# Kernel optimization log

Measured on AMD Instinct MI355X. Metric: run time of the kernel, lower is better.

## Reference

```python
import jax, jax.numpy as jnp
import numpy as np

HIDDEN = 1024
HEADS = 16
HEAD_DIM = HIDDEN // HEADS


def setup_inputs() -> dict:
    key = jax.random.key(0)
    k1, k2, k3, k4 = jax.random.split(key, 4)
    x = jax.random.normal(k1, (4, 2048, HIDDEN), dtype=jnp.float32)
    # qkv: Linear(hidden, 3*hidden, bias=False) -> weight [3*hidden, hidden]
    w_qkv = jax.random.normal(k2, (3 * HIDDEN, HIDDEN), dtype=jnp.float32) * (HIDDEN ** -0.5)
    # out_proj: Linear(hidden, hidden) with bias
    w_out = jax.random.normal(k3, (HIDDEN, HIDDEN), dtype=jnp.float32) * (HIDDEN ** -0.5)
    b_out = jax.random.normal(k4, (HIDDEN,), dtype=jnp.float32) * 0.01
    return {"x": x, "w_qkv": w_qkv, "w_out": w_out, "b_out": b_out}


def reference(x, w_qkv, w_out, b_out):
    B, N, _ = x.shape
    scale = HEAD_DIM ** -0.5
    qkv = jnp.einsum('bnc,dc->bnd', x, w_qkv)            # [B,N,3*hidden]
    qkv = qkv.reshape(B, N, 3, HEADS, HEAD_DIM)
    qkv = jnp.transpose(qkv, (2, 0, 3, 1, 4))            # [3,B,H,N,hd]
    q, k, v = qkv[0], qkv[1], qkv[2]
    att = jnp.einsum('bhxd,bhyd->bhxy', q, k) * scale    # [B,H,N,N]
    att = jax.nn.softmax(att, axis=-1)
    out = jnp.einsum('bhxy,bhyd->bhxd', att, v)          # [B,H,N,hd]
    out = jnp.transpose(out, (0, 2, 1, 3)).reshape(B, N, HIDDEN)
    out = jnp.einsum('bnc,dc->bnd', out, w_out) + b_out
    return out
```

## Files before the change

kernel.cpp:

```cpp
#include <hip/hip_runtime.h>

typedef unsigned short u16;
typedef short short8 __attribute__((ext_vector_type(8)));
typedef float f32x4 __attribute__((ext_vector_type(4)));
typedef float f32x16 __attribute__((ext_vector_type(16)));
typedef unsigned short u16x4 __attribute__((ext_vector_type(4)));
typedef unsigned int u32x4 __attribute__((ext_vector_type(4)));

#define MFMA16(a, b, c) __builtin_amdgcn_mfma_f32_16x16x32_bf16((a), (b), (c), 0, 0, 0)
#define MFMA32(a, b, c) __builtin_amdgcn_mfma_f32_32x32x16_bf16((a), (b), (c), 0, 0, 0)

#if __has_builtin(__builtin_amdgcn_exp2f)
#define EXP2F(x) __builtin_amdgcn_exp2f(x)
#else
#define EXP2F(x) exp2f(x)
#endif

__device__ __forceinline__ u16 f2bf(float f) {
    unsigned u = __builtin_bit_cast(unsigned, f);
    u += 0x7FFFu + ((u >> 16) & 1u);
    return (u16)(u >> 16);
}

__device__ __forceinline__ void async16(void* lds, const void* g) {
    __builtin_amdgcn_global_load_lds(
        (const __attribute__((address_space(1))) void*)g,
        (__attribute__((address_space(3))) void*)lds, 16, 0, 0);
}

__device__ __forceinline__ unsigned cvtpk(float lo, float hi) {
    unsigned r;
    asm("v_cvt_pk_bf16_f32 %0, %1, %2" : "=v"(r) : "v"(lo), "v"(hi));
    return r;
}
__device__ __forceinline__ void plswap(unsigned& a, unsigned& b) {
    asm("v_permlane32_swap_b32 %0, %1" : "+v"(a), "+v"(b));
}

__device__ __forceinline__ void packP(const f32x16& s, short8& f0, short8& f1) {
    u32x4 u0, u1;
    {
        unsigned a = cvtpk(s[0], s[1]), b = cvtpk(s[4], s[5]);
        plswap(a, b);
        unsigned c = cvtpk(s[2], s[3]), d = cvtpk(s[6], s[7]);
        plswap(c, d);
        u0[0] = a; u0[1] = c; u0[2] = b; u0[3] = d;
    }
    {
        unsigned a = cvtpk(s[8], s[9]), b = cvtpk(s[12], s[13]);
        plswap(a, b);
        unsigned c = cvtpk(s[10], s[11]), d = cvtpk(s[14], s[15]);
        plswap(c, d);
        u1[0] = a; u1[1] = c; u1[2] = b; u1[3] = d;
    }
    f0 = __builtin_bit_cast(short8, u0);
    f1 = __builtin_bit_cast(short8, u1);
}

__global__ __launch_bounds__(256) void cast3(const float* __restrict__ x,
                                             const float* __restrict__ wqkv,
                                             const float* __restrict__ wout,
                                             u16* __restrict__ dst) {
    const int blk = blockIdx.x;
    const float* src;
    int idx;
    float sc = 1.0f;
    u16* out;
    if (blk < 8192) {
        src = x; out = dst; idx = (blk * 256 + threadIdx.x) * 4;
    } else if (blk < 11264) {
        src = wqkv; out = dst + (size_t)8192 * 1024;
        idx = ((blk - 8192) * 256 + threadIdx.x) * 4;
        if (idx < 1024 * 1024) sc = 0.18033688011112042f;
    } else {
        src = wout; out = dst + (size_t)11264 * 1024;
        idx = ((blk - 11264) * 256 + threadIdx.x) * 4;
    }
    float4 v = *(const float4*)(src + idx);
    u16x4 r;
    r[0] = f2bf(v.x * sc); r[1] = f2bf(v.y * sc);
    r[2] = f2bf(v.z * sc); r[3] = f2bf(v.w * sc);
    *(u16x4*)(out + idx) = r;
}

__global__ __launch_bounds__(512, 2) void gemm256(const u16* __restrict__ A,
                                                  const u16* __restrict__ B,
                                                  u16* __restrict__ qk) {
    __shared__ u16 lds[2][2][16384];
    const int tid = threadIdx.x;
    const int l = tid & 63;
    const int w = tid >> 6;
    const int g = l >> 4, lo = l & 15;
    const int wrow = w >> 2, wcol = w & 3;
    const int xcd = blockIdx.x & 7, j = blockIdx.x >> 3;
    const int tm = xcd * 4 + (j & 3), tn = j >> 2;
    const int rowBase = tm << 8, colBase = tn << 8;

    const int srow = tid >> 3;
    const int scol = (((tid * 16) ^ (((tid >> 3) & 7) << 4)) & 127) >> 1;
    const u16* pa = A + (size_t)(rowBase + srow) * 1024 + scol;
    const u16* pb = B + (size_t)(colBase + srow) * 1024 + scol;
    const int ldsOff = tid * 16;

    int abase[2], bbase[2];
#pragma unroll
    for (int k = 0; k < 2; ++k) {
        abase[k] = (((wrow * 128 + lo) * 128 + k * 64 + g * 16) ^ ((lo & 7) << 4));
        bbase[k] = (((wcol * 64 + lo) * 128 + k * 64 + g * 16) ^ ((lo & 7) << 4));
    }

    f32x4 acc[8][4] = {};

#define STAGE256(buf, kt)                                                                   \
    {                                                                                       \
        const u16* sa = pa + (kt) * 64;                                                     \
        const u16* sb = pb + (kt) * 64;                                                     \
        _Pragma("unroll")                                                                   \
        for (int i = 0; i < 4; ++i) {                                                       \
            async16((char*)lds[buf][0] + ldsOff + i * 8192, sa + (size_t)i * 64 * 1024);    \
            async16((char*)lds[buf][1] + ldsOff + i * 8192, sb + (size_t)i * 64 * 1024);    \
        }                                                                                   \
    }

    STAGE256(0, 0);
    __syncthreads();

    for (int kt = 0; kt < 16; ++kt) {
        const int cur = kt & 1;
        if (kt < 15) STAGE256(cur ^ 1, kt + 1);
        const char* la = (const char*)lds[cur][0];
        const char* lb = (const char*)lds[cur][1];

        short8 bf[4][2], af[4][2];
#pragma unroll
        for (int n = 0; n < 4; ++n)
#pragma unroll
            for (int k = 0; k < 2; ++k)
                bf[n][k] = *(const short8*)(lb + bbase[k] + n * 2048);
#pragma unroll
        for (int m = 0; m < 4; ++m)
#pragma unroll
            for (int k = 0; k < 2; ++k)
                af[m][k] = *(const short8*)(la + abase[k] + m * 2048);
        __builtin_amdgcn_s_setprio(1);
#pragma unroll
        for (int m = 0; m < 4; ++m)
#pragma unroll
            for (int n = 0; n < 4; ++n) {
                acc[m][n] = MFMA16(af[m][0], bf[n][0], acc[m][n]);
                acc[m][n] = MFMA16(af[m][1], bf[n][1], acc[m][n]);
            }
        __builtin_amdgcn_s_setprio(0);
#pragma unroll
        for (int m = 0; m < 4; ++m)
#pragma unroll
            for (int k = 0; k < 2; ++k)
                af[m][k] = *(const short8*)(la + abase[k] + (m + 4) * 2048);
        __builtin_amdgcn_s_setprio(1);
#pragma unroll
        for (int m = 0; m < 4; ++m)
#pragma unroll
            for (int n = 0; n < 4; ++n) {
                acc[m + 4][n] = MFMA16(af[m][0], bf[n][0], acc[m + 4][n]);
                acc[m + 4][n] = MFMA16(af[m][1], bf[n][1], acc[m + 4][n]);
            }
        __builtin_amdgcn_s_setprio(0);
        __syncthreads();
    }
#undef STAGE256

#pragma unroll
    for (int n = 0; n < 4; ++n) {
        const int c = colBase + wcol * 64 + n * 16 + lo;
#pragma unroll
        for (int m = 0; m < 8; ++m) {
            const int r0 = rowBase + wrow * 128 + m * 16 + g * 4;
#pragma unroll
            for (int i = 0; i < 4; ++i)
                qk[(size_t)(r0 + i) * 2048 + c] = f2bf(acc[m][n][i]);
        }
    }
}

__global__ __launch_bounds__(256, 2) void gemmV(const u16* __restrict__ A,
                                                const u16* __restrict__ Bv,
                                                u16* __restrict__ vt) {
    __shared__ u16 As[128 * 64];
    __shared__ u16 Bs[128 * 64];
    const int tid = threadIdx.x;
    const int w = tid >> 6, l = tid & 63;
    const int g = l >> 4, lo = l & 15;
    const int xcd = blockIdx.x & 7, j = blockIdx.x >> 3;
    const int tm = xcd * 8 + (j & 7), tn = j >> 3;
    const int rowBase = tm << 7, colBase = tn << 7;
    const int wrow = w >> 1, wcol = w & 1;

    const int srow = tid >> 3;
    const int scol = (((tid * 16) ^ (((tid >> 3) & 7) << 4)) & 127) >> 1;
    const u16* pa = A + (size_t)(rowBase + srow) * 1024 + scol;
    const u16* pb = Bv + (size_t)(colBase + srow) * 1024 + scol;
    const int ldsOff = tid * 16;

    int abase[2], bbase[2];
#pragma unroll
    for (int k = 0; k < 2; ++k) {
        abase[k] = (((wrow * 64 + lo) * 128 + k * 64 + g * 16) ^ ((lo & 7) << 4));
        bbase[k] = (((wcol * 64 + lo) * 128 + k * 64 + g * 16) ^ ((lo & 7) << 4));
    }

    f32x4 acc[4][4] = {};

    for (int kt = 0; kt < 16; ++kt) {
        const int kbase = kt * 64;
#pragma unroll
        for (int i = 0; i < 4; ++i) {
            async16((char*)As + ldsOff + i * 4096, pa + kbase + (size_t)i * 32 * 1024);
            async16((char*)Bs + ldsOff + i * 4096, pb + kbase + (size_t)i * 32 * 1024);
        }
        __syncthreads();
        short8 af[4][2], bf[4][2];
#pragma unroll
        for (int mi = 0; mi < 4; ++mi)
#pragma unroll
            for (int k = 0; k < 2; ++k)
                af[mi][k] = *(const short8*)((const char*)As + abase[k] + mi * 2048);
#pragma unroll
        for (int ni = 0; ni < 4; ++ni)
#pragma unroll
            for (int k = 0; k < 2; ++k)
                bf[ni][k] = *(const short8*)((const char*)Bs + bbase[k] + ni * 2048);
        __builtin_amdgcn_s_setprio(1);
#pragma unroll
        for (int mi = 0; mi < 4; ++mi)
#pragma unroll
            for (int ni = 0; ni < 4; ++ni) {
                acc[mi][ni] = MFMA16(af[mi][0], bf[ni][0], acc[mi][ni]);
                acc[mi][ni] = MFMA16(af[mi][1], bf[ni][1], acc[mi][ni]);
            }
        __builtin_amdgcn_s_setprio(0);
        __syncthreads();
    }

    const int b = rowBase >> 11;
#pragma unroll
    for (int ni = 0; ni < 4; ++ni) {
        const int c = colBase + wcol * 64 + ni * 16 + lo;
        const int hh = c >> 6, d = c & 63;
        u16* vrow = vt + ((size_t)((b * 16 + hh) * 64 + d)) * 2048;
#pragma unroll
        for (int mi = 0; mi < 4; ++mi) {
            const int r0 = rowBase + wrow * 64 + mi * 16 + g * 4;
            u16x4 pk;
#pragma unroll
            for (int i = 0; i < 4; ++i) pk[i] = f2bf(acc[mi][ni][i]);
            *(u16x4*)(vrow + (r0 & 2047)) = pk;
        }
    }
}

__global__ __launch_bounds__(256, 2) void gemm_bt(const u16* __restrict__ A,
                                                  const u16* __restrict__ B,
                                                  float* __restrict__ Cf,
                                                  const float* __restrict__ bias,
                                                  int M, int N, int K) {
    __shared__ u16 As[128 * 64];
    __shared__ u16 Bs[128 * 64];
    const int tid = threadIdx.x;
    const int w = tid >> 6, l = tid & 63;
    const int g = l >> 4, lo = l & 15;
    const int mtiles = M >> 7;
    const int S = mtiles >> 3;
    const int xcd = blockIdx.x & 7, j = blockIdx.x >> 3;
    const int tm = xcd * S + (j % S), tn = j / S;
    const int rowBase = tm << 7, colBase = tn << 7;
    const int wrow = w >> 1, wcol = w & 1;

    const int srow = tid >> 3;
    const int scol = (((tid * 16) ^ (((tid >> 3) & 7) << 4)) & 127) >> 1;
    const u16* pa = A + (size_t)(rowBase + srow) * K + scol;
    const u16* pb = B + (size_t)(colBase + srow) * K + scol;
    const int ldsOff = tid * 16;

    int abase[2], bbase[2];
#pragma unroll
    for (int k = 0; k < 2; ++k) {
        abase[k] = (((wrow * 64 + lo) * 128 + k * 64 + g * 16) ^ ((lo & 7) << 4));
        bbase[k] = (((wcol * 64 + lo) * 128 + k * 64 + g * 16) ^ ((lo & 7) << 4));
    }

    f32x4 acc[4][4] = {};

    const int nk = K >> 6;
    for (int kt = 0; kt < nk; ++kt) {
        const int kbase = kt * 64;
#pragma unroll
        for (int i = 0; i < 4; ++i) {
            async16((char*)As + ldsOff + i * 4096, pa + kbase + (size_t)i * 32 * K);
            async16((char*)Bs + ldsOff + i * 4096, pb + kbase + (size_t)i * 32 * K);
        }
        __syncthreads();
        short8 af[4][2], bf[4][2];
#pragma unroll
        for (int mi = 0; mi < 4; ++mi)
#pragma unroll
            for (int k = 0; k < 2; ++k)
                af[mi][k] = *(const short8*)((const char*)As + abase[k] + mi * 2048);
#pragma unroll
        for (int ni = 0; ni < 4; ++ni)
#pragma unroll
            for (int k = 0; k < 2; ++k)
                bf[ni][k] = *(const short8*)((const char*)Bs + bbase[k] + ni * 2048);
        __builtin_amdgcn_s_setprio(1);
#pragma unroll
        for (int mi = 0; mi < 4; ++mi)
#pragma unroll
            for (int ni = 0; ni < 4; ++ni) {
                acc[mi][ni] = MFMA16(af[mi][0], bf[ni][0], acc[mi][ni]);
                acc[mi][ni] = MFMA16(af[mi][1], bf[ni][1], acc[mi][ni]);
            }
        __builtin_amdgcn_s_setprio(0);
        __syncthreads();
    }

#pragma unroll
    for (int ni = 0; ni < 4; ++ni) {
        const int c = colBase + wcol * 64 + ni * 16 + lo;
        const float bv = bias[c];
#pragma unroll
        for (int mi = 0; mi < 4; ++mi) {
            const int r0 = rowBase + wrow * 64 + mi * 16 + g * 4;
#pragma unroll
            for (int i = 0; i < 4; ++i)
                Cf[(size_t)(r0 + i) * N + c] = acc[mi][ni][i] + bv;
        }
    }
}

__global__ __launch_bounds__(256, 2) void attn_fwd(const u16* __restrict__ qkb,
                                                   const u16* __restrict__ vtg,
                                                   u16* __restrict__ outb) {
    __shared__ u16 Ks[2][2][4096];
    __shared__ u16 Vs[2][2][4096];
    const int tid = threadIdx.x;
    const int w = tid >> 6, l = tid & 63;
    const int hi = l >> 5, lq = l & 31;

    const int lin = (blockIdx.x & 7) * 64 + (blockIdx.x >> 3);
    const int bh = lin >> 3, qt = lin & 7;
    const int b = bh >> 4, h = bh & 15;
    const size_t rowQ0 = (size_t)b * 2048 + qt * 256 + w * 32;
    const size_t rowQ1 = rowQ0 + 128;

    short8 qf0[4], qf1[4];
#pragma unroll
    for (int ks = 0; ks < 4; ++ks) {
        qf0[ks] = *(const short8*)(qkb + (rowQ0 + lq) * 2048 + h * 64 + ks * 16 + hi * 8);
        qf1[ks] = *(const short8*)(qkb + (rowQ1 + lq) * 2048 + h * 64 + ks * 16 + hi * 8);
    }

    int koff[4];
#pragma unroll
    for (int ks = 0; ks < 4; ++ks)
        koff[ks] = (lq * 128 + ks * 32 + hi * 16) ^ ((lq & 7) << 4);

    const int L0 = tid * 16, L1 = tid * 16 + 4096;
    const int kr0 = L0 >> 7, kc0 = ((L0 ^ ((kr0 & 7) << 4)) & 127) >> 1;
    const int kr1 = L1 >> 7, kc1 = ((L1 ^ ((kr1 & 7) << 4)) & 127) >> 1;
    const u16* ks0 = qkb + (size_t)(b * 2048 + kr0) * 2048 + 1024 + h * 64 + kc0;
    const u16* ks1 = qkb + (size_t)(b * 2048 + kr1) * 2048 + 1024 + h * 64 + kc1;
    const u16* vs0 = vtg + ((size_t)bh * 64 + kr0) * 2048 + kc0;
    const u16* vs1 = vtg + ((size_t)bh * 64 + kr1) * 2048 + kc1;
    const size_t KADV = (size_t)128 * 2048;
    const size_t CADV = (size_t)64 * 2048;

    f32x16 O00, O01, Ol0, O10, O11, Ol1;
#pragma unroll
    for (int i = 0; i < 16; ++i) {
        O00[i] = 0.f; O01[i] = 0.f; Ol0[i] = 0.f;
        O10[i] = 0.f; O11[i] = 0.f; Ol1[i] = 0.f;
    }
    const f32x16 Z = {};
    const short8 onesv = {16256, 16256, 16256, 16256, 16256, 16256, 16256, 16256};

#define STAGEKV(buf)                                                        \
    {                                                                       \
        async16((char*)Ks[buf][0] + L0, ks0);                               \
        async16((char*)Ks[buf][0] + L1, ks1);                               \
        async16((char*)Ks[buf][1] + L0, ks0 + CADV);                        \
        async16((char*)Ks[buf][1] + L1, ks1 + CADV);                        \
        async16((char*)Vs[buf][0] + L0, vs0);                               \
        async16((char*)Vs[buf][0] + L1, vs1);                               \
        async16((char*)Vs[buf][1] + L0, vs0 + 64);                          \
        async16((char*)Vs[buf][1] + L1, vs1 + 64);                          \
        ks0 += KADV; ks1 += KADV; vs0 += 128; vs1 += 128;                   \
    }

    STAGEKV(0);

    int cur = 0;
    for (int kt = 0; kt < 16; ++kt) {
        __syncthreads();
        if (kt < 15) STAGEKV(cur ^ 1);

#pragma unroll
        for (int c = 0; c < 2; ++c) {
            const char* kb = (const char*)Ks[cur][c];
            const char* vb = (const char*)Vs[cur][c];

#pragma unroll
            for (int t = 0; t < 2; ++t) {
                const int tb = t * 4096;
                short8 kf0 = *(const short8*)(kb + koff[0] + tb);
                short8 kf1 = *(const short8*)(kb + koff[1] + tb);
                short8 kf2 = *(const short8*)(kb + koff[2] + tb);
                short8 kf3 = *(const short8*)(kb + koff[3] + tb);
                short8 vfa = *(const short8*)(vb + koff[t * 2]);
                short8 vfb = *(const short8*)(vb + koff[t * 2] + 4096);
                short8 vfc = *(const short8*)(vb + koff[t * 2 + 1]);
                short8 vfd = *(const short8*)(vb + koff[t * 2 + 1] + 4096);

                {
                    __builtin_amdgcn_s_setprio(1);
                    f32x16 s = MFMA32(kf0, qf0[0], Z);
                    s = MFMA32(kf1, qf0[1], s);
                    s = MFMA32(kf2, qf0[2], s);
                    s = MFMA32(kf3, qf0[3], s);
                    __builtin_amdgcn_s_setprio(0);
#pragma unroll
                    for (int i = 0; i < 16; ++i) s[i] = EXP2F(s[i]);
                    short8 p0, p1;
                    packP(s, p0, p1);
                    __builtin_amdgcn_s_setprio(1);
                    Ol0 = MFMA32(p0, onesv, Ol0);
                    Ol0 = MFMA32(p1, onesv, Ol0);
                    O00 = MFMA32(p0, vfa, O00);
                    O01 = MFMA32(p0, vfb, O01);
                    O00 = MFMA32(p1, vfc, O00);
                    O01 = MFMA32(p1, vfd, O01);
                    __builtin_amdgcn_s_setprio(0);
                }
                {
                    __builtin_amdgcn_s_setprio(1);
                    f32x16 s = MFMA32(kf0, qf1[0], Z);
                    s = MFMA32(kf1, qf1[1], s);
                    s = MFMA32(kf2, qf1[2], s);
                    s = MFMA32(kf3, qf1[3], s);
                    __builtin_amdgcn_s_setprio(0);
#pragma unroll
                    for (int i = 0; i < 16; ++i) s[i] = EXP2F(s[i]);
                    short8 p0, p1;
                    packP(s, p0, p1);
                    __builtin_amdgcn_s_setprio(1);
                    Ol1 = MFMA32(p0, onesv, Ol1);
                    Ol1 = MFMA32(p1, onesv, Ol1);
                    O10 = MFMA32(p0, vfa, O10);
                    O11 = MFMA32(p0, vfb, O11);
                    O10 = MFMA32(p1, vfc, O10);
                    O11 = MFMA32(p1, vfd, O11);
                    __builtin_amdgcn_s_setprio(0);
                }
            }
        }
        cur ^= 1;
    }
#undef STAGEKV

#pragma unroll
    for (int r = 0; r < 16; ++r) {
        const int qrow = (r & 3) + 8 * (r >> 2) + 4 * hi;
        {
            const float linv = 1.0f / Ol0[r];
            u16* op = outb + (rowQ0 + qrow) * 1024 + h * 64 + lq;
            op[0] = f2bf(O00[r] * linv);
            op[32] = f2bf(O01[r] * linv);
        }
        {
            const float linv = 1.0f / Ol1[r];
            u16* op = outb + (rowQ1 + qrow) * 1024 + h * 64 + lq;
            op[0] = f2bf(O10[r] * linv);
            op[32] = f2bf(O11[r] * linv);
        }
    }
}

extern "C" void kernel_launch(void* const* d_in, const int* in_sizes, int n_in,
                              void* d_out, int out_size, void* d_ws, size_t ws_size,
                              hipStream_t stream) {
    const float* x     = (const float*)d_in[0];
    const float* w_qkv = (const float*)d_in[1];
    const float* w_out = (const float*)d_in[2];
    const float* b_out = (const float*)d_in[3];
    float* out = (float*)d_out;

    u16* xb    = (u16*)d_ws;
    u16* wqkvb = xb    + (size_t)8192 * 1024;
    u16* woutb = wqkvb + (size_t)3072 * 1024;
    u16* qkb   = woutb + (size_t)1024 * 1024;
    u16* vtg   = qkb   + (size_t)8192 * 2048;
    u16* attb  = vtg   + (size_t)64 * 64 * 2048;

    cast3<<<12288, 256, 0, stream>>>(x, w_qkv, w_out, xb);

    gemm256<<<256, 512, 0, stream>>>(xb, wqkvb, qkb);
    gemmV<<<512, 256, 0, stream>>>(xb, wqkvb + (size_t)2048 * 1024, vtg);

    attn_fwd<<<512, 256, 0, stream>>>(qkb, vtg, attb);

    gemm_bt<<<dim3((8192 / 128) * (1024 / 128)), 256, 0, stream>>>(
        attb, woutb, out, b_out, 8192, 1024, 1024);
}
```

Baseline: 170.8 us.

## Merge Q/K and V projections into one double-buffered 128x128 GEMM kernel

Replaces the separate 256x256 QK GEMM and 128x128 V GEMM with a single 1536-block 128x128 kernel. It branches in the epilogue to write either the row-major QK output or the transposed V layout. The unified QKV kernel and the output-projection GEMM now double-buffer their LDS tiles, so the next K-slice loads while the current one computes. This removes a kernel launch and the per-iteration load stall, but smaller tiles lower the arithmetic intensity for the QK part and double the LDS per block.

After: 173.8 us. No clear change (+1.8%).

```diff
diff --git a/kernel.cpp b/kernel.cpp
--- a/kernel.cpp
+++ b/kernel.cpp
@@ -83,110 +83,12 @@
     *(u16x4*)(out + idx) = r;
 }
 
-__global__ __launch_bounds__(512, 2) void gemm256(const u16* __restrict__ A,
+__global__ __launch_bounds__(256, 2) void gemmQKV(const u16* __restrict__ A,
                                                   const u16* __restrict__ B,
-                                                  u16* __restrict__ qk) {
-    __shared__ u16 lds[2][2][16384];
-    const int tid = threadIdx.x;
-    const int l = tid & 63;
-    const int w = tid >> 6;
-    const int g = l >> 4, lo = l & 15;
-    const int wrow = w >> 2, wcol = w & 3;
-    const int xcd = blockIdx.x & 7, j = blockIdx.x >> 3;
-    const int tm = xcd * 4 + (j & 3), tn = j >> 2;
-    const int rowBase = tm << 8, colBase = tn << 8;
-
-    const int srow = tid >> 3;
-    const int scol = (((tid * 16) ^ (((tid >> 3) & 7) << 4)) & 127) >> 1;
-    const u16* pa = A + (size_t)(rowBase + srow) * 1024 + scol;
-    const u16* pb = B + (size_t)(colBase + srow) * 1024 + scol;
-    const int ldsOff = tid * 16;
-
-    int abase[2], bbase[2];
-#pragma unroll
-    for (int k = 0; k < 2; ++k) {
-        abase[k] = (((wrow * 128 + lo) * 128 + k * 64 + g * 16) ^ ((lo & 7) << 4));
-        bbase[k] = (((wcol * 64 + lo) * 128 + k * 64 + g * 16) ^ ((lo & 7) << 4));
-    }
-
-    f32x4 acc[8][4] = {};
-
-#define STAGE256(buf, kt)                                                                   \
-    {                                                                                       \
-        const u16* sa = pa + (kt) * 64;                                                     \
-        const u16* sb = pb + (kt) * 64;                                                     \
-        _Pragma("unroll")                                                                   \
-        for (int i = 0; i < 4; ++i) {                                                       \
-            async16((char*)lds[buf][0] + ldsOff + i * 8192, sa + (size_t)i * 64 * 1024);    \
-            async16((char*)lds[buf][1] + ldsOff + i * 8192, sb + (size_t)i * 64 * 1024);    \
-        }                                                                                   \
-    }
-
-    STAGE256(0, 0);
-    __syncthreads();
-
-    for (int kt = 0; kt < 16; ++kt) {
-        const int cur = kt & 1;
-        if (kt < 15) STAGE256(cur ^ 1, kt + 1);
-        const char* la = (const char*)lds[cur][0];
-        const char* lb = (const char*)lds[cur][1];
-
-        short8 bf[4][2], af[4][2];
-#pragma unroll
-        for (int n = 0; n < 4; ++n)
-#pragma unroll
-            for (int k = 0; k < 2; ++k)
-                bf[n][k] = *(const short8*)(lb + bbase[k] + n * 2048);
-#pragma unroll
-        for (int m = 0; m < 4; ++m)
-#pragma unroll
-            for (int k = 0; k < 2; ++k)
-                af[m][k] = *(const short8*)(la + abase[k] + m * 2048);
-        __builtin_amdgcn_s_setprio(1);
-#pragma unroll
-        for (int m = 0; m < 4; ++m)
-#pragma unroll
-            for (int n = 0; n < 4; ++n) {
-                acc[m][n] = MFMA16(af[m][0], bf[n][0], acc[m][n]);
-                acc[m][n] = MFMA16(af[m][1], bf[n][1], acc[m][n]);
-            }
-        __builtin_amdgcn_s_setprio(0);
-#pragma unroll
-        for (int m = 0; m < 4; ++m)
-#pragma unroll
-            for (int k = 0; k < 2; ++k)
-                af[m][k] = *(const short8*)(la + abase[k] + (m + 4) * 2048);
-        __builtin_amdgcn_s_setprio(1);
-#pragma unroll
-        for (int m = 0; m < 4; ++m)
-#pragma unroll
-            for (int n = 0; n < 4; ++n) {
-                acc[m + 4][n] = MFMA16(af[m][0], bf[n][0], acc[m + 4][n]);
-                acc[m + 4][n] = MFMA16(af[m][1], bf[n][1], acc[m + 4][n]);
-            }
-        __builtin_amdgcn_s_setprio(0);
-        __syncthreads();
-    }
-#undef STAGE256
-
-#pragma unroll
-    for (int n = 0; n < 4; ++n) {
-        const int c = colBase + wcol * 64 + n * 16 + lo;
-#pragma unroll
-        for (int m = 0; m < 8; ++m) {
-            const int r0 = rowBase + wrow * 128 + m * 16 + g * 4;
-#pragma unroll
-            for (int i = 0; i < 4; ++i)
-                qk[(size_t)(r0 + i) * 2048 + c] = f2bf(acc[m][n][i]);
-        }
-    }
-}
-
-__global__ __launch_bounds__(256, 2) void gemmV(const u16* __restrict__ A,
-                                                const u16* __restrict__ Bv,
-                                                u16* __restrict__ vt) {
-    __shared__ u16 As[128 * 64];
-    __shared__ u16 Bs[128 * 64];
+                                                  u16* __restrict__ qk,
+                                                  u16* __restrict__ vt) {
+    __shared__ u16 As[2][128 * 64];
+    __shared__ u16 Bs[2][128 * 64];
     const int tid = threadIdx.x;
     const int w = tid >> 6, l = tid & 63;
     const int g = l >> 4, lo = l & 15;
@@ -198,7 +100,7 @@
     const int srow = tid >> 3;
     const int scol = (((tid * 16) ^ (((tid >> 3) & 7) << 4)) & 127) >> 1;
     const u16* pa = A + (size_t)(rowBase + srow) * 1024 + scol;
-    const u16* pb = Bv + (size_t)(colBase + srow) * 1024 + scol;
+    const u16* pb = B + (size_t)(colBase + srow) * 1024 + scol;
     const int ldsOff = tid * 16;
 
     int abase[2], bbase[2];
@@ -210,25 +112,36 @@
 
     f32x4 acc[4][4] = {};
 
+#define STAGEQKV(buf, kt)                                                                  \
+    {                                                                                      \
+        const int kb_ = (kt) * 64;                                                         \
+        _Pragma("unroll")                                                                  \
+        for (int i = 0; i < 4; ++i) {                                                      \
+            async16((char*)As[buf] + ldsOff + i * 4096, pa + kb_ + (size_t)i * 32 * 1024); \
+            async16((char*)Bs[buf] + ldsOff + i * 4096, pb + kb_ + (size_t)i * 32 * 1024); \
+        }                                                                                  \
+    }
+
+    STAGEQKV(0, 0);
+    __syncthreads();
+
     for (int kt = 0; kt < 16; ++kt) {
-        const int kbase = kt * 64;
-#pragma unroll
-        for (int i = 0; i < 4; ++i) {
-            async16((char*)As + ldsOff + i * 4096, pa + kbase + (size_t)i * 32 * 1024);
-            async16((char*)Bs + ldsOff + i * 4096, pb + kbase + (size_t)i * 32 * 1024);
-        }
-        __syncthreads();
+        const int cur = kt & 1;
+        if (kt < 15) STAGEQKV(cur ^ 1, kt + 1);
+        const char* la = (const char*)As[cur];
+        const char* lb = (const char*)Bs[cur];
+
         short8 af[4][2], bf[4][2];
 #pragma unroll
         for (int mi = 0; mi < 4; ++mi)
 #pragma unroll
             for (int k = 0; k < 2; ++k)
-                af[mi][k] = *(const short8*)((const char*)As + abase[k] + mi * 2048);
+                af[mi][k] = *(const short8*)(la + abase[k] + mi * 2048);
 #pragma unroll
         for (int ni = 0; ni < 4; ++ni)
 #pragma unroll
             for (int k = 0; k < 2; ++k)
-                bf[ni][k] = *(const short8*)((const char*)Bs + bbase[k] + ni * 2048);
+                bf[ni][k] = *(const short8*)(lb + bbase[k] + ni * 2048);
         __builtin_amdgcn_s_setprio(1);
 #pragma unroll
         for (int mi = 0; mi < 4; ++mi)
@@ -240,20 +153,35 @@
         __builtin_amdgcn_s_setprio(0);
         __syncthreads();
     }
-
-    const int b = rowBase >> 11;
-#pragma unroll
-    for (int ni = 0; ni < 4; ++ni) {
-        const int c = colBase + wcol * 64 + ni * 16 + lo;
-        const int hh = c >> 6, d = c & 63;
-        u16* vrow = vt + ((size_t)((b * 16 + hh) * 64 + d)) * 2048;
-#pragma unroll
-        for (int mi = 0; mi < 4; ++mi) {
-            const int r0 = rowBase + wrow * 64 + mi * 16 + g * 4;
-            u16x4 pk;
-#pragma unroll
-            for (int i = 0; i < 4; ++i) pk[i] = f2bf(acc[mi][ni][i]);
-            *(u16x4*)(vrow + (r0 & 2047)) = pk;
+#undef STAGEQKV
+
+    if (colBase < 2048) {
+#pragma unroll
+        for (int ni = 0; ni < 4; ++ni) {
+            const int c = colBase + wcol * 64 + ni * 16 + lo;
+#pragma unroll
+            for (int mi = 0; mi < 4; ++mi) {
+                const int r0 = rowBase + wrow * 64 + mi * 16 + g * 4;
+#pragma unroll
+                for (int i = 0; i < 4; ++i)
+                    qk[(size_t)(r0 + i) * 2048 + c] = f2bf(acc[mi][ni][i]);
+            }
+        }
+    } else {
+        const int b = rowBase >> 11;
+#pragma unroll
+        for (int ni = 0; ni < 4; ++ni) {
+            const int c = colBase + wcol * 64 + ni * 16 + lo;
+            const int hh = (c - 2048) >> 6, d = (c - 2048) & 63;
+            u16* vrow = vt + ((size_t)((b * 16 + hh) * 64 + d)) * 2048;
+#pragma unroll
+            for (int mi = 0; mi < 4; ++mi) {
+                const int r0 = rowBase + wrow * 64 + mi * 16 + g * 4;
+                u16x4 pk;
+#pragma unroll
+                for (int i = 0; i < 4; ++i) pk[i] = f2bf(acc[mi][ni][i]);
+                *(u16x4*)(vrow + (r0 & 2047)) = pk;
+            }
         }
     }
 }
@@ -263,8 +191,8 @@
                                                   float* __restrict__ Cf,
                                                   const float* __restrict__ bias,
                                                   int M, int N, int K) {
-    __shared__ u16 As[128 * 64];
-    __shared__ u16 Bs[128 * 64];
+    __shared__ u16 As[2][128 * 64];
+    __shared__ u16 Bs[2][128 * 64];
     const int tid = threadIdx.x;
     const int w = tid >> 6, l = tid & 63;
     const int g = l >> 4, lo = l & 15;
@@ -290,26 +218,37 @@
 
     f32x4 acc[4][4] = {};
 
+#define STAGE2(buf, kt)                                                                 \
+    {                                                                                   \
+        const int kb_ = (kt) * 64;                                                      \
+        _Pragma("unroll")                                                               \
+        for (int i = 0; i < 4; ++i) {                                                   \
+            async16((char*)As[buf] + ldsOff + i * 4096, pa + kb_ + (size_t)i * 32 * K); \
+            async16((char*)Bs[buf] + ldsOff + i * 4096, pb + kb_ + (size_t)i * 32 * K); \
+        }                                                                               \
+    }
+
     const int nk = K >> 6;
+    STAGE2(0, 0);
+    __syncthreads();
+
     for (int kt = 0; kt < nk; ++kt) {
-        const int kbase = kt * 64;
-#pragma unroll
-        for (int i = 0; i < 4; ++i) {
-            async16((char*)As + ldsOff + i * 4096, pa + kbase + (size_t)i * 32 * K);
-            async16((char*)Bs + ldsOff + i * 4096, pb + kbase + (size_t)i * 32 * K);
-        }
-        __syncthreads();
+        const int cur = kt & 1;
+        if (kt < nk - 1) STAGE2(cur ^ 1, kt + 1);
+        const char* la = (const char*)As[cur];
+        const char* lb = (const char*)Bs[cur];
+
         short8 af[4][2], bf[4][2];
 #pragma unroll
         for (int mi = 0; mi < 4; ++mi)
 #pragma unroll
             for (int k = 0; k < 2; ++k)
-                af[mi][k] = *(const short8*)((const char*)As + abase[k] + mi * 2048);
+                af[mi][k] = *(const short8*)(la + abase[k] + mi * 2048);
 #pragma unroll
         for (int ni = 0; ni < 4; ++ni)
 #pragma unroll
             for (int k = 0; k < 2; ++k)
-                bf[ni][k] = *(const short8*)((const char*)Bs + bbase[k] + ni * 2048);
+                bf[ni][k] = *(const short8*)(lb + bbase[k] + ni * 2048);
         __builtin_amdgcn_s_setprio(1);
 #pragma unroll
         for (int mi = 0; mi < 4; ++mi)
@@ -321,6 +260,7 @@
         __builtin_amdgcn_s_setprio(0);
         __syncthreads();
     }
+#undef STAGE2
 
 #pragma unroll
     for (int ni = 0; ni < 4; ++ni) {
@@ -501,11 +441,10 @@
 
     cast3<<<12288, 256, 0, stream>>>(x, w_qkv, w_out, xb);
 
-    gemm256<<<256, 512, 0, stream>>>(xb, wqkvb, qkb);
-    gemmV<<<512, 256, 0, stream>>>(xb, wqkvb + (size_t)2048 * 1024, vtg);
+    gemmQKV<<<1536, 256, 0, stream>>>(xb, wqkvb, qkb, vtg);
 
     attn_fwd<<<512, 256, 0, stream>>>(qkb, vtg, attb);
 
-    gemm_bt<<<dim3((8192 / 128) * (1024 / 128)), 256, 0, stream>>>(
+    gemm_bt<<<dim3(512), 256, 0, stream>>>(
         attb, woutb, out, b_out, 8192, 1024, 1024);
 }
```

## Replace 256x256 double-buffered QK GEMM with 128x128 single-buffered tiles

Applied to the files above, without the earlier changes.

The Q/K projection GEMM goes from 256x256 tiles with 512 threads and double-buffered async LDS loads to 128x128 tiles with 256 threads and a single LDS buffer that is loaded and synced every k-step. The grid grows from 256 to 1024 blocks, which should spread work over more CUs and lower register and LDS pressure per block. In exchange it gives up load/compute overlap and halves data reuse per tile. The gemm_bt grid is now written as a literal 512, which equals the old expression.

Result: no change. 173.4 us (+1.6%).

```diff
diff --git a/kernel.cpp b/kernel.cpp
--- a/kernel.cpp
+++ b/kernel.cpp
@@ -83,18 +83,18 @@
     *(u16x4*)(out + idx) = r;
 }
 
-__global__ __launch_bounds__(512, 2) void gemm256(const u16* __restrict__ A,
-                                                  const u16* __restrict__ B,
-                                                  u16* __restrict__ qk) {
-    __shared__ u16 lds[2][2][16384];
+__global__ __launch_bounds__(256, 2) void gemmQK(const u16* __restrict__ A,
+                                                 const u16* __restrict__ B,
+                                                 u16* __restrict__ qk) {
+    __shared__ u16 As[128 * 64];
+    __shared__ u16 Bs[128 * 64];
     const int tid = threadIdx.x;
-    const int l = tid & 63;
-    const int w = tid >> 6;
+    const int w = tid >> 6, l = tid & 63;
     const int g = l >> 4, lo = l & 15;
-    const int wrow = w >> 2, wcol = w & 3;
     const int xcd = blockIdx.x & 7, j = blockIdx.x >> 3;
-    const int tm = xcd * 4 + (j & 3), tn = j >> 2;
-    const int rowBase = tm << 8, colBase = tn << 8;
+    const int tm = xcd * 8 + (j & 7), tn = j >> 3;
+    const int rowBase = tm << 7, colBase = tn << 7;
+    const int wrow = w >> 1, wcol = w & 1;
 
     const int srow = tid >> 3;
     const int scol = (((tid * 16) ^ (((tid >> 3) & 7) << 4)) & 127) >> 1;
@@ -105,79 +105,52 @@
     int abase[2], bbase[2];
 #pragma unroll
     for (int k = 0; k < 2; ++k) {
-        abase[k] = (((wrow * 128 + lo) * 128 + k * 64 + g * 16) ^ ((lo & 7) << 4));
+        abase[k] = (((wrow * 64 + lo) * 128 + k * 64 + g * 16) ^ ((lo & 7) << 4));
         bbase[k] = (((wcol * 64 + lo) * 128 + k * 64 + g * 16) ^ ((lo & 7) << 4));
     }
 
-    f32x4 acc[8][4] = {};
-
-#define STAGE256(buf, kt)                                                                   \
-    {                                                                                       \
-        const u16* sa = pa + (kt) * 64;                                                     \
-        const u16* sb = pb + (kt) * 64;                                                     \
-        _Pragma("unroll")                                                                   \
-        for (int i = 0; i < 4; ++i) {                                                       \
-            async16((char*)lds[buf][0] + ldsOff + i * 8192, sa + (size_t)i * 64 * 1024);    \
-            async16((char*)lds[buf][1] + ldsOff + i * 8192, sb + (size_t)i * 64 * 1024);    \
-        }                                                                                   \
-    }
-
-    STAGE256(0, 0);
-    __syncthreads();
+    f32x4 acc[4][4] = {};
 
     for (int kt = 0; kt < 16; ++kt) {
-        const int cur = kt & 1;
-        if (kt < 15) STAGE256(cur ^ 1, kt + 1);
-        const char* la = (const char*)lds[cur][0];
-        const char* lb = (const char*)lds[cur][1];
-
-        short8 bf[4][2], af[4][2];
-#pragma unroll
-        for (int n = 0; n < 4; ++n)
-#pragma unroll
-            for (int k = 0; k < 2; ++k)
-                bf[n][k] = *(const short8*)(lb + bbase[k] + n * 2048);
-#pragma unroll
-        for (int m = 0; m < 4; ++m)
-#pragma unroll
-            for (int k = 0; k < 2; ++k)
-                af[m][k] = *(const short8*)(la + abase[k] + m * 2048);
+        const int kbase = kt * 64;
+#pragma unroll
+        for (int i = 0; i < 4; ++i) {
+            async16((char*)As + ldsOff + i * 4096, pa + kbase + (size_t)i * 32 * 1024);
+            async16((char*)Bs + ldsOff + i * 4096, pb + kbase + (size_t)i * 32 * 1024);
+        }
+        __syncthreads();
+        short8 af[4][2], bf[4][2];
+#pragma unroll
+        for (int mi = 0; mi < 4; ++mi)
+#pragma unroll
+            for (int k = 0; k < 2; ++k)
+                af[mi][k] = *(const short8*)((const char*)As + abase[k] + mi * 2048);
+#pragma unroll
+        for (int ni = 0; ni < 4; ++ni)
+#pragma unroll
+            for (int k = 0; k < 2; ++k)
+                bf[ni][k] = *(const short8*)((const char*)Bs + bbase[k] + ni * 2048);
         __builtin_amdgcn_s_setprio(1);
 #pragma unroll
-        for (int m = 0; m < 4; ++m)
-#pragma unroll
-            for (int n = 0; n < 4; ++n) {
-                acc[m][n] = MFMA16(af[m][0], bf[n][0], acc[m][n]);
-                acc[m][n] = MFMA16(af[m][1], bf[n][1], acc[m][n]);
+        for (int mi = 0; mi < 4; ++mi)
+#pragma unroll
+            for (int ni = 0; ni < 4; ++ni) {
+                acc[mi][ni] = MFMA16(af[mi][0], bf[ni][0], acc[mi][ni]);
+                acc[mi][ni] = MFMA16(af[mi][1], bf[ni][1], acc[mi][ni]);
             }
         __builtin_amdgcn_s_setprio(0);
-#pragma unroll
-        for (int m = 0; m < 4; ++m)
-#pragma unroll
-            for (int k = 0; k < 2; ++k)
-                af[m][k] = *(const short8*)(la + abase[k] + (m + 4) * 2048);
-        __builtin_amdgcn_s_setprio(1);
-#pragma unroll
-        for (int m = 0; m < 4; ++m)
-#pragma unroll
-            for (int n = 0; n < 4; ++n) {
-                acc[m + 4][n] = MFMA16(af[m][0], bf[n][0], acc[m + 4][n]);
-                acc[m + 4][n] = MFMA16(af[m][1], bf[n][1], acc[m + 4][n]);
-            }
-        __builtin_amdgcn_s_setprio(0);
-        __syncthreads();
-    }
-#undef STAGE256
-
-#pragma unroll
-    for (int n = 0; n < 4; ++n) {
-        const int c = colBase + wcol * 64 + n * 16 + lo;
-#pragma unroll
-        for (int m = 0; m < 8; ++m) {
-            const int r0 = rowBase + wrow * 128 + m * 16 + g * 4;
+        __syncthreads();
+    }
+
+#pragma unroll
+    for (int ni = 0; ni < 4; ++ni) {
+        const int c = colBase + wcol * 64 + ni * 16 + lo;
+#pragma unroll
+        for (int mi = 0; mi < 4; ++mi) {
+            const int r0 = rowBase + wrow * 64 + mi * 16 + g * 4;
 #pragma unroll
             for (int i = 0; i < 4; ++i)
-                qk[(size_t)(r0 + i) * 2048 + c] = f2bf(acc[m][n][i]);
+                qk[(size_t)(r0 + i) * 2048 + c] = f2bf(acc[mi][ni][i]);
         }
     }
 }
@@ -501,11 +474,11 @@
 
     cast3<<<12288, 256, 0, stream>>>(x, w_qkv, w_out, xb);
 
-    gemm256<<<256, 512, 0, stream>>>(xb, wqkvb, qkb);
+    gemmQK<<<1024, 256, 0, stream>>>(xb, wqkvb, qkb);
     gemmV<<<512, 256, 0, stream>>>(xb, wqkvb + (size_t)2048 * 1024, vtg);
 
     attn_fwd<<<512, 256, 0, stream>>>(qkb, vtg, attb);
 
-    gemm_bt<<<dim3((8192 / 128) * (1024 / 128)), 256, 0, stream>>>(
+    gemm_bt<<<dim3(512), 256, 0, stream>>>(
         attb, woutb, out, b_out, 8192, 1024, 1024);
 }
```
